# Kernel tuning notes

Hardware: AMD Instinct MI355X
Metric: run time of the kernel (lower is better)

Reference implementation:

```python
import jax, jax.numpy as jnp
import numpy as np

B, D, K = 32768, 512, 5
SIM_THRESH = 0.7
GATE_TEMP = 1.0
LN_EPS = 1e-5


def setup_inputs() -> dict:
    key = jax.random.key(0)
    ks = jax.random.split(key, 12)
    s = 1.0 / np.sqrt(D)
    query = jax.random.normal(ks[0], (B, D), dtype=jnp.float32)
    retrieved_memories = jax.random.normal(ks[1], (B, K, D), dtype=jnp.float32)
    similarities = jax.random.uniform(ks[2], (B, K), dtype=jnp.float32)
    mask = jax.random.randint(ks[3], (B, K), 0, 2) > 0
    mask = mask.at[:, 0].set(True)  # at least one valid memory per row
    return {
        "query": query,
        "retrieved_memories": retrieved_memories,
        "similarities": similarities,
        "mask": mask,
        "Wq": jax.random.normal(ks[4], (D, D), dtype=jnp.float32) * s,
        "bq": jnp.zeros((D,), jnp.float32),
        "Wk": jax.random.normal(ks[5], (D, D), dtype=jnp.float32) * s,
        "bk": jnp.zeros((D,), jnp.float32),
        "Wv": jax.random.normal(ks[6], (D, D), dtype=jnp.float32) * s,
        "bv": jnp.zeros((D,), jnp.float32),
        "Wo": jax.random.normal(ks[7], (D, D), dtype=jnp.float32) * s,
        "bo": jnp.zeros((D,), jnp.float32),
        "Wg": jax.random.normal(ks[8], (2 * D, 1), dtype=jnp.float32) * s,
        "bg": jnp.zeros((1,), jnp.float32),
        "ln_g": jnp.ones((D,), jnp.float32),
        "ln_b": jnp.zeros((D,), jnp.float32),
    }


def reference(query, retrieved_memories, similarities, mask,
              Wq, bq, Wk, bk, Wv, bv, Wo, bo, Wg, bg, ln_g, ln_b):
    scale = D ** (-0.5)
    q = query @ Wq + bq                                          # (B, D)
    k = jnp.einsum('bkd,de->bke', retrieved_memories, Wk) + bk   # (B, K, D)
    v = jnp.einsum('bkd,de->bke', retrieved_memories, Wv) + bv   # (B, K, D)
    scores = jnp.einsum('bd,bkd->bk', q, k) * scale              # (B, K)
    scores = jnp.where(mask, scores, -jnp.inf)
    w = jax.nn.softmax(scores, axis=-1)
    w = jnp.where(mask, w, 0.0)
    mem = jnp.einsum('bk,bkd->bd', w, v)                         # (B, D)
    mem = mem @ Wo + bo
    # gated fusion
    max_sim = jnp.max(similarities, axis=-1, keepdims=True)      # (B, 1)
    gate = jax.nn.sigmoid(jnp.concatenate([query, mem], axis=-1) @ Wg + bg)
    conf = jax.nn.sigmoid(GATE_TEMP * (max_sim - SIM_THRESH))
    out = query + (gate * conf) * mem
    # layer norm
    mu = jnp.mean(out, axis=-1, keepdims=True)
    var = jnp.mean((out - mu) ** 2, axis=-1, keepdims=True)
    out = (out - mu) * jax.lax.rsqrt(var + LN_EPS) * ln_g + ln_b
    return out
```

## Files before the change

### kernel.cpp

```cpp
#include <hip/hip_runtime.h>

#define DD 512
#define KM 5
#define B_ROWS 32768

typedef __attribute__((ext_vector_type(8))) short short8;
typedef __attribute__((ext_vector_type(4))) short s16x4;
typedef __attribute__((ext_vector_type(4))) float f32x4;

static __device__ __forceinline__ short f2bf(float x) {
  unsigned u = __builtin_bit_cast(unsigned, x);
  u = (u + 0x7fffu + ((u >> 16) & 1u)) >> 16;
  return (short)u;
}
static __device__ __forceinline__ float bf2f(short s) {
  unsigned u = ((unsigned)(unsigned short)s) << 16;
  return __builtin_bit_cast(float, u);
}

#define SYNC0() do { asm volatile("s_waitcnt vmcnt(0) lgkmcnt(0)" ::: "memory"); __builtin_amdgcn_s_barrier(); } while (0)
#define SYNC2() do { asm volatile("s_waitcnt vmcnt(2) lgkmcnt(0)" ::: "memory"); __builtin_amdgcn_s_barrier(); } while (0)
#define BAR_LGKM() do { asm volatile("s_waitcnt lgkmcnt(0)" ::: "memory"); __builtin_amdgcn_s_barrier(); } while (0)

__global__ __launch_bounds__(512, 2)
void prepG(const float* __restrict__ Wq, const float* __restrict__ bq,
           const float* __restrict__ Wk, const float* __restrict__ Wv,
           const float* __restrict__ Wo, const float* __restrict__ bo,
           const float* __restrict__ bv,
           short* __restrict__ At, short* __restrict__ Ct,
           float* __restrict__ w0, float* __restrict__ d0) {
  __shared__ short sh[12288];
  const int tid = threadIdx.x;
  const int blk = blockIdx.x;
  if (blk < 64) {
    const bool isC = blk >= 32;
    const int b = blk & 31;
    const int j0 = (b >> 3) * 128;
    const int i0 = (b & 7) * 64;
    const int lane = tid & 63;
    const int w = tid >> 6;
    const int wm = w & 1, wn = w >> 1;
    const int kg = lane >> 4, lr = lane & 15;
    const float* Ysrc = isC ? Wv : Wq;
    f32x4 acc[4] = {};
    f32x4 ra0, ra1;
    f32x4 rbv;
    if (!isC) {
      const float* p = Wk + (size_t)(j0 + (tid >> 2)) * DD + (tid & 3) * 8;
      ra0 = *(const f32x4*)p; ra1 = *(const f32x4*)(p + 4);
    } else {
      const float* p = Wo + (size_t)(tid >> 4) * DD + j0 + (tid & 15) * 8;
      ra0 = *(const f32x4*)p; ra1 = *(const f32x4*)(p + 4);
    }
    rbv = *(const f32x4*)(Ysrc + (size_t)(i0 + (tid >> 3)) * DD + (tid & 7) * 4);
    for (int ki = 0; ki < 16; ++ki) {
      short* As = (ki & 1) ? (sh + 4096) : sh;
      short* Bs = (ki & 1) ? (sh + 10240) : (sh + 8192);
      if (!isC) {
        short8 sv;
        sv[0]=f2bf(ra0[0]); sv[1]=f2bf(ra0[1]); sv[2]=f2bf(ra0[2]); sv[3]=f2bf(ra0[3]);
        sv[4]=f2bf(ra1[0]); sv[5]=f2bf(ra1[1]); sv[6]=f2bf(ra1[2]); sv[7]=f2bf(ra1[3]);
        *(short8*)&As[(tid >> 2) * 32 + (((tid & 3) * 8) ^ (((tid >> 2) & 3) << 3))] = sv;
      } else {
        const int e = tid >> 4;
#pragma unroll
        for (int c = 0; c < 8; ++c) {
          const int j = (tid & 15) * 8 + c;
          const float v = (c < 4) ? ra0[c & 3] : ra1[c & 3];
          As[j * 32 + (e ^ ((j & 3) << 3))] = f2bf(v);
        }
      }
      {
        s16x4 sv;
        sv[0]=f2bf(rbv[0]); sv[1]=f2bf(rbv[1]); sv[2]=f2bf(rbv[2]); sv[3]=f2bf(rbv[3]);
        *(s16x4*)&Bs[(tid >> 3) * 32 + (((tid & 7) * 4) ^ (((tid >> 3) & 3) << 3))] = sv;
      }
      if (ki < 15) {
        const int kt = (ki + 1) * 32;
        if (!isC) {
          const float* p = Wk + (size_t)(j0 + (tid >> 2)) * DD + kt + (tid & 3) * 8;
          ra0 = *(const f32x4*)p; ra1 = *(const f32x4*)(p + 4);
        } else {
          const float* p = Wo + (size_t)(kt + (tid >> 4)) * DD + j0 + (tid & 15) * 8;
          ra0 = *(const f32x4*)p; ra1 = *(const f32x4*)(p + 4);
        }
        rbv = *(const f32x4*)(Ysrc + (size_t)(i0 + (tid >> 3)) * DD + kt + (tid & 7) * 4);
      }
      __syncthreads();
      short8 av[4], bvv;
#pragma unroll
      for (int mi = 0; mi < 4; ++mi) {
        const int ar = wm * 64 + mi * 16 + lr;
        av[mi] = *(const short8*)&As[ar * 32 + ((kg * 8) ^ ((lr & 3) << 3))];
      }
      {
        const int br = wn * 16 + lr;
        bvv = *(const short8*)&Bs[br * 32 + ((kg * 8) ^ ((lr & 3) << 3))];
      }
#pragma unroll
      for (int mi = 0; mi < 4; ++mi)
        acc[mi] = __builtin_amdgcn_mfma_f32_16x16x32_bf16(av[mi], bvv, acc[mi], 0, 0, 0);
      __syncthreads();
    }
    short* P = isC ? Ct : At;
    const int col = i0 + wn * 16 + lr;
#pragma unroll
    for (int mi = 0; mi < 4; ++mi)
#pragma unroll
      for (int r = 0; r < 4; ++r)
        P[(size_t)(j0 + wm * 64 + mi * 16 + kg * 4 + r) * DD + col] = f2bf(acc[mi][r]);
  } else if (blk < 128) {
    const int j = (blk - 64) * 8 + (tid >> 6);
    const int lane = tid & 63;
    const float* r = Wk + (size_t)j * DD + lane * 8;
    f32x4 a = *(const f32x4*)r;
    f32x4 c = *(const f32x4*)(r + 4);
    const float* bp = bq + lane * 8;
    f32x4 ba = *(const f32x4*)bp;
    f32x4 bc = *(const f32x4*)(bp + 4);
    float s = a[0]*ba[0] + a[1]*ba[1] + a[2]*ba[2] + a[3]*ba[3]
            + c[0]*bc[0] + c[1]*bc[1] + c[2]*bc[2] + c[3]*bc[3];
#pragma unroll
    for (int off = 32; off > 0; off >>= 1) s += __shfl_xor(s, off);
    if (lane == 0) w0[j] = s;
  } else {
    float* red = (float*)sh;
    const int j = (blk - 128) * 256 + (tid & 255);
    const int half = tid >> 8;
    float s = 0.f;
    for (int e = half * 256; e < half * 256 + 256; ++e)
      s += bv[e] * Wo[(size_t)e * DD + j];
    red[half * 256 + (tid & 255)] = s;
    __syncthreads();
    if (half == 0) d0[j] = red[tid] + red[256 + tid] + bo[j];
  }
}

#define STAGE_W(MAT, TI, DST) do {                                                 \
  _Pragma("unroll") for (int c = 0; c < 4; ++c) {                                  \
    const short* _src = (MAT) + (size_t)(c * 128 + (tid >> 2)) * DD + (TI) * 32    \
                        + (((tid & 3) * 8) ^ (((tid >> 2) & 3) << 3));             \
    __builtin_amdgcn_global_load_lds(                                              \
        (const __attribute__((address_space(1))) void*)_src,                       \
        (__attribute__((address_space(3))) void*)(&(DST)[c * 4096 + w * 512]),     \
        16, 0, 0);                                                                 \
  } } while (0)

#define WRITE_A(DST, QLO, QHI) do {                                                \
  short8 _sv;                                                                      \
  _sv[0]=f2bf((QLO)[0]); _sv[1]=f2bf((QLO)[1]); _sv[2]=f2bf((QLO)[2]); _sv[3]=f2bf((QLO)[3]); \
  _sv[4]=f2bf((QHI)[0]); _sv[5]=f2bf((QHI)[1]); _sv[6]=f2bf((QHI)[2]); _sv[7]=f2bf((QHI)[3]); \
  *(short8*)&(DST)[arow * 32 + (acol ^ ((arow & 3) << 3))] = _sv; } while (0)

#define ROW_FINISH(SV, MA, MC, VM, ROW)                                     \
    {                                                                       \
      float mx = -1e30f;                                                    \
      _Pragma("unroll") for (int k = 0; k < KM; ++k)                        \
        if ((VM) & (1 << k)) mx = fmaxf(mx, SV[k]);                         \
      float wk[KM]; float sum = 0.f;                                        \
      _Pragma("unroll") for (int k = 0; k < KM; ++k) {                      \
        wk[k] = ((VM) & (1 << k)) ? __expf(SV[k] - mx) : 0.f;               \
        sum += wk[k];                                                       \
      }                                                                     \
      const float inv = 1.f / sum;                                          \
      float o[8] = {0.f,0.f,0.f,0.f,0.f,0.f,0.f,0.f};                       \
      _Pragma("unroll") for (int k = 0; k < KM; ++k)                        \
        if ((VM) & (1 << k)) {                                              \
          const float g = wk[k] * inv;                                      \
          _Pragma("unroll") for (int i = 0; i < 4; ++i) {                   \
            o[i] += g * MA[k][i]; o[4 + i] += g * MC[k][i];                 \
          }                                                                 \
        }                                                                   \
      short8 ov;                                                            \
      _Pragma("unroll") for (int i = 0; i < 8; ++i) ov[i] = f2bf(o[i]);     \
      *(short8*)&R1[((ROW) * DD + lane * 8) ^ (((ROW) & 7) << 3)] = ov;     \
    }

__global__ __launch_bounds__(512, 2)
void mk(const float* __restrict__ q, const short* __restrict__ Atw,
        const float* __restrict__ w0, const float* __restrict__ mem,
        const int* __restrict__ mask, const short* __restrict__ Ctw,
        const float* __restrict__ d0, const float* __restrict__ sims,
        const float* __restrict__ Wg, const float* __restrict__ bgp,
        const float* __restrict__ lng, const float* __restrict__ lnb,
        float* __restrict__ outp) {
  __shared__ short R1[128 * DD];
  __shared__ short RS[DD * 32];
  const int tid = threadIdx.x;
  const int lane = tid & 63;
  const int w = tid >> 6;
  const int kg = lane >> 4, lr = lane & 15;
  const int bm = blockIdx.x;

  short* As0 = R1;
  short* As1 = R1 + 4096;
  short* RS1 = R1 + 8192;

  f32x4 acc[8][4] = {};
  const int arow = tid >> 2, acol = (tid & 3) * 8;
  const float* qbase = q + (size_t)(bm * 128 + arow) * DD + acol;
  {
    STAGE_W(Atw, 0, RS);
    __builtin_amdgcn_sched_barrier(0);
    f32x4 q0a = *(const f32x4*)qbase;
    f32x4 q0b = *(const f32x4*)(qbase + 4);
    WRITE_A(As0, q0a, q0b);
    f32x4 qA = *(const f32x4*)(qbase + 32);
    f32x4 qB = *(const f32x4*)(qbase + 36);
    SYNC2();
    for (int ki = 0; ki < 16; ++ki) {
      const short* Asc = (ki & 1) ? As1 : As0;
      short* Asn = (ki & 1) ? As0 : As1;
      const short* RSc = (ki & 1) ? RS1 : RS;
      short* RSn = (ki & 1) ? RS : RS1;
      short8 av[8], bvv[4];
#pragma unroll
      for (int mi = 0; mi < 8; ++mi) {
        const int ar = mi * 16 + lr;
        av[mi] = *(const short8*)&Asc[ar * 32 + ((kg * 8) ^ ((lr & 3) << 3))];
      }
#pragma unroll
      for (int ni = 0; ni < 4; ++ni) {
        const int row = w * 64 + ni * 16 + lr;
        bvv[ni] = *(const short8*)&RSc[row * 32 + ((kg * 8) ^ ((lr & 3) << 3))];
      }
      if (ki < 15) {
        WRITE_A(Asn, qA, qB);
        STAGE_W(Atw, ki + 1, RSn);
        __builtin_amdgcn_sched_barrier(0);
        if (ki < 14) {
          qA = *(const f32x4*)(qbase + (ki + 2) * 32);
          qB = *(const f32x4*)(qbase + (ki + 2) * 32 + 4);
        }
      }
#pragma unroll
      for (int mi = 0; mi < 8; ++mi)
#pragma unroll
        for (int ni = 0; ni < 4; ++ni)
          acc[mi][ni] = __builtin_amdgcn_mfma_f32_16x16x32_bf16(av[mi], bvv[ni], acc[mi][ni], 0, 0, 0);
      if (ki < 14) { SYNC2(); } else { SYNC0(); }
    }
  }
#pragma unroll
  for (int ni = 0; ni < 4; ++ni) {
    const int col = w * 64 + ni * 16 + lr;
    const float b0 = w0[col];
#pragma unroll
    for (int mi = 0; mi < 8; ++mi)
#pragma unroll
      for (int r = 0; r < 4; ++r)
        R1[(mi * 16 + kg * 4 + r) * DD + col] = f2bf(acc[mi][ni][r] + b0);
  }
  BAR_LGKM();
  STAGE_W(Ctw, 0, RS);
  const float scale = 0.044194173824159216f;
  for (int rr = 0; rr < 16; rr += 2) {
    const int row0 = w * 16 + rr;
    const size_t b0 = (size_t)bm * 128 + row0;
    const short8 tv0 = *(const short8*)&R1[row0 * DD + lane * 8];
    const short8 tv1 = *(const short8*)&R1[(row0 + 1) * DD + lane * 8];
    float tf0[8], tf1[8];
#pragma unroll
    for (int i = 0; i < 8; ++i) { tf0[i] = bf2f(tv0[i]); tf1[i] = bf2f(tv1[i]); }
    int vm0 = 0, vm1 = 0;
#pragma unroll
    for (int k = 0; k < KM; ++k) {
      vm0 |= (__builtin_amdgcn_readfirstlane(mask[b0 * KM + k]) ? 1 : 0) << k;
      vm1 |= (__builtin_amdgcn_readfirstlane(mask[(b0 + 1) * KM + k]) ? 1 : 0) << k;
    }
    f32x4 ma0[KM], mc0[KM], ma1[KM], mc1[KM];
#pragma unroll
    for (int k = 0; k < KM; ++k) {
      if (vm0 & (1 << k)) {
        const f32x4* mp = (const f32x4*)(mem + (b0 * KM + k) * DD + lane * 8);
        ma0[k] = __builtin_nontemporal_load(mp);
        mc0[k] = __builtin_nontemporal_load(mp + 1);
      }
      if (vm1 & (1 << k)) {
        const f32x4* mp = (const f32x4*)(mem + ((b0 + 1) * KM + k) * DD + lane * 8);
        ma1[k] = __builtin_nontemporal_load(mp);
        mc1[k] = __builtin_nontemporal_load(mp + 1);
      }
    }
    float s0[KM], s1[KM];
#pragma unroll
    for (int k = 0; k < KM; ++k) {
      if (vm0 & (1 << k)) {
        float p = 0.f;
#pragma unroll
        for (int i = 0; i < 4; ++i) { p += tf0[i] * ma0[k][i]; p += tf0[4 + i] * mc0[k][i]; }
#pragma unroll
        for (int off = 32; off > 0; off >>= 1) p += __shfl_xor(p, off);
        s0[k] = p * scale;
      }
      if (vm1 & (1 << k)) {
        float p = 0.f;
#pragma unroll
        for (int i = 0; i < 4; ++i) { p += tf1[i] * ma1[k][i]; p += tf1[4 + i] * mc1[k][i]; }
#pragma unroll
        for (int off = 32; off > 0; off >>= 1) p += __shfl_xor(p, off);
        s1[k] = p * scale;
      }
    }
    ROW_FINISH(s0, ma0, mc0, vm0, row0)
    ROW_FINISH(s1, ma1, mc1, vm1, (row0 + 1))
  }
  SYNC0();
  f32x4 acc2[8][4] = {};
  for (int ki = 0; ki < 16; ++ki) {
    short8 av[8], bvv[4];
#pragma unroll
    for (int mi = 0; mi < 8; ++mi) {
      const int ar = mi * 16 + lr;
      av[mi] = *(const short8*)&R1[(ar * DD + ki * 32 + kg * 8) ^ ((ar & 7) << 3)];
    }
#pragma unroll
    for (int ni = 0; ni < 4; ++ni) {
      const int row = w * 64 + ni * 16 + lr;
      bvv[ni] = *(const short8*)&RS[row * 32 + ((kg * 8) ^ ((lr & 3) << 3))];
    }
    BAR_LGKM();
    if (ki < 15) STAGE_W(Ctw, ki + 1, RS);
#pragma unroll
    for (int mi = 0; mi < 8; ++mi)
#pragma unroll
      for (int ni = 0; ni < 4; ++ni)
        acc2[mi][ni] = __builtin_amdgcn_mfma_f32_16x16x32_bf16(av[mi], bvv[ni], acc2[mi][ni], 0, 0, 0);
    SYNC0();
  }
#pragma unroll
  for (int ni = 0; ni < 4; ++ni) {
    const int col = w * 64 + ni * 16 + lr;
    const float b0 = d0[col];
#pragma unroll
    for (int mi = 0; mi < 8; ++mi)
#pragma unroll
      for (int r = 0; r < 4; ++r)
        R1[(mi * 16 + kg * 4 + r) * DD + col] = f2bf(acc2[mi][ni][r] + b0);
  }
  BAR_LGKM();
  {
    const float* wg1 = Wg + lane * 8;
    const float* wg2 = Wg + DD + lane * 8;
    f32x4 g1a = *(const f32x4*)wg1, g1b = *(const f32x4*)(wg1 + 4);
    f32x4 g2a = *(const f32x4*)wg2, g2b = *(const f32x4*)(wg2 + 4);
    f32x4 la = *(const f32x4*)(lng + lane * 8), lb4 = *(const f32x4*)(lng + lane * 8 + 4);
    f32x4 ba = *(const f32x4*)(lnb + lane * 8), bb4 = *(const f32x4*)(lnb + lane * 8 + 4);
    const float bgs = bgp[0];
    for (int rr = 0; rr < 16; ++rr) {
      const int row = w * 16 + rr;
      const size_t b = (size_t)bm * 128 + row;
      const float* qp = q + b * DD + lane * 8;
      f32x4 q0 = *(const f32x4*)qp;
      f32x4 q1 = *(const f32x4*)(qp + 4);
      float qf[8] = {q0[0],q0[1],q0[2],q0[3],q1[0],q1[1],q1[2],q1[3]};
      const short8 mv = *(const short8*)&R1[row * DD + lane * 8];
      float mf[8];
#pragma unroll
      for (int i = 0; i < 8; ++i) mf[i] = bf2f(mv[i]);
      float gp = qf[0]*g1a[0]+qf[1]*g1a[1]+qf[2]*g1a[2]+qf[3]*g1a[3]
               + qf[4]*g1b[0]+qf[5]*g1b[1]+qf[6]*g1b[2]+qf[7]*g1b[3]
               + mf[0]*g2a[0]+mf[1]*g2a[1]+mf[2]*g2a[2]+mf[3]*g2a[3]
               + mf[4]*g2b[0]+mf[5]*g2b[1]+mf[6]*g2b[2]+mf[7]*g2b[3];
#pragma unroll
      for (int off = 32; off > 0; off >>= 1) gp += __shfl_xor(gp, off);
      const float gate = 1.f / (1.f + __expf(-(gp + bgs)));
      float ms = sims[b * KM];
#pragma unroll
      for (int k = 1; k < KM; ++k) ms = fmaxf(ms, sims[b * KM + k]);
      const float conf = 1.f / (1.f + __expf(-(ms - 0.7f)));
      const float gc = gate * conf;
      float o[8];
      float s1 = 0.f, s2 = 0.f;
#pragma unroll
      for (int i = 0; i < 8; ++i) {
        o[i] = qf[i] + gc * mf[i];
        s1 += o[i];
        s2 += o[i] * o[i];
      }
#pragma unroll
      for (int off = 32; off > 0; off >>= 1) { s1 += __shfl_xor(s1, off); s2 += __shfl_xor(s2, off); }
      const float mu = s1 * (1.f / 512.f);
      const float var = s2 * (1.f / 512.f) - mu * mu;
      const float rs = rsqrtf(var + 1e-5f);
      f32x4 r0, r1;
#pragma unroll
      for (int i = 0; i < 4; ++i) r0[i] = (o[i] - mu) * rs * la[i] + ba[i];
#pragma unroll
      for (int i = 0; i < 4; ++i) r1[i] = (o[4 + i] - mu) * rs * lb4[i] + bb4[i];
      float* op = outp + b * DD + lane * 8;
      __builtin_nontemporal_store(r0, (f32x4*)op);
      __builtin_nontemporal_store(r1, (f32x4*)(op + 4));
    }
  }
}

extern "C" void kernel_launch(void* const* d_in, const int* in_sizes, int n_in,
                              void* d_out, int out_size, void* d_ws, size_t ws_size,
                              hipStream_t stream) {
  const float* query = (const float*)d_in[0];
  const float* mem   = (const float*)d_in[1];
  const float* sims  = (const float*)d_in[2];
  const int*   mask  = (const int*)d_in[3];
  const float* Wq = (const float*)d_in[4];
  const float* bq = (const float*)d_in[5];
  const float* Wk = (const float*)d_in[6];
  const float* Wv = (const float*)d_in[8];
  const float* bv = (const float*)d_in[9];
  const float* Wo = (const float*)d_in[10];
  const float* bo = (const float*)d_in[11];
  const float* Wg = (const float*)d_in[12];
  const float* bg = (const float*)d_in[13];
  const float* ln_g = (const float*)d_in[14];
  const float* ln_b = (const float*)d_in[15];
  float* out = (float*)d_out;

  char* ws = (char*)d_ws;
  short* At = (short*)ws;
  short* Ct = At + (size_t)DD * DD;
  float* w0 = (float*)(Ct + (size_t)DD * DD);
  float* d0 = w0 + DD;

  prepG<<<dim3(130), dim3(512), 0, stream>>>(Wq, bq, Wk, Wv, Wo, bo, bv, At, Ct, w0, d0);
  mk<<<dim3(B_ROWS / 128), dim3(512), 0, stream>>>(query, At, w0, mem, mask,
                                                   Ct, d0, sims, Wg, bg, ln_g, ln_b, out);
}
```

Measured before the change: 147.6 us.

## Load B weight fragments directly from global into registers, drop LDS staging

The prep kernel now writes the precomputed At/Ct weight products in a K-tiled packed layout, so each lane's MFMA B fragment is one contiguous 16-byte global load. The main kernel drops the RS LDS buffer and the global_load_lds staging. Instead it double-buffers B fragments in registers, with loops unrolled in pairs, and uses lighter LDS-only barriers. This removes LDS traffic and vmcnt waits for the weights, but relies on L2/L1 hits for the repeated weight reads across blocks and raises register pressure.

```diff
diff --git a/kernel.cpp b/kernel.cpp
--- a/kernel.cpp
+++ b/kernel.cpp
@@ -18,8 +18,6 @@
   return __builtin_bit_cast(float, u);
 }
 
-#define SYNC0() do { asm volatile("s_waitcnt vmcnt(0) lgkmcnt(0)" ::: "memory"); __builtin_amdgcn_s_barrier(); } while (0)
-#define SYNC2() do { asm volatile("s_waitcnt vmcnt(2) lgkmcnt(0)" ::: "memory"); __builtin_amdgcn_s_barrier(); } while (0)
 #define BAR_LGKM() do { asm volatile("s_waitcnt lgkmcnt(0)" ::: "memory"); __builtin_amdgcn_s_barrier(); } while (0)
 
 __global__ __launch_bounds__(512, 2)
@@ -103,12 +101,16 @@
       __syncthreads();
     }
     short* P = isC ? Ct : At;
-    const int col = i0 + wn * 16 + lr;
+    const int cwl = wn * 16 + lr;
+    const int kiv = (b & 7) * 2 + (cwl >> 5);
+    const int kkv = cwl & 31;
 #pragma unroll
     for (int mi = 0; mi < 4; ++mi)
 #pragma unroll
-      for (int r = 0; r < 4; ++r)
-        P[(size_t)(j0 + wm * 64 + mi * 16 + kg * 4 + r) * DD + col] = f2bf(acc[mi][r]);
+      for (int r = 0; r < 4; ++r) {
+        const int j = j0 + wm * 64 + mi * 16 + kg * 4 + r;
+        P[(size_t)kiv * 16384 + j * 32 + kkv] = f2bf(acc[mi][r]);
+      }
   } else if (blk < 128) {
     const int j = (blk - 64) * 8 + (tid >> 6);
     const int lane = tid & 63;
@@ -136,21 +138,47 @@
   }
 }
 
-#define STAGE_W(MAT, TI, DST) do {                                                 \
-  _Pragma("unroll") for (int c = 0; c < 4; ++c) {                                  \
-    const short* _src = (MAT) + (size_t)(c * 128 + (tid >> 2)) * DD + (TI) * 32    \
-                        + (((tid & 3) * 8) ^ (((tid >> 2) & 3) << 3));             \
-    __builtin_amdgcn_global_load_lds(                                              \
-        (const __attribute__((address_space(1))) void*)_src,                       \
-        (__attribute__((address_space(3))) void*)(&(DST)[c * 4096 + w * 512]),     \
-        16, 0, 0);                                                                 \
-  } } while (0)
-
 #define WRITE_A(DST, QLO, QHI) do {                                                \
   short8 _sv;                                                                      \
   _sv[0]=f2bf((QLO)[0]); _sv[1]=f2bf((QLO)[1]); _sv[2]=f2bf((QLO)[2]); _sv[3]=f2bf((QLO)[3]); \
   _sv[4]=f2bf((QHI)[0]); _sv[5]=f2bf((QHI)[1]); _sv[6]=f2bf((QHI)[2]); _sv[7]=f2bf((QHI)[3]); \
   *(short8*)&(DST)[arow * 32 + (acol ^ ((arow & 3) << 3))] = _sv; } while (0)
+
+#define G1ITER(KI, ASC, ASN, BC, BN) do {                                   \
+    short8 av[8];                                                           \
+    _Pragma("unroll") for (int mi = 0; mi < 8; ++mi) {                      \
+      const int ar = mi * 16 + lr;                                          \
+      av[mi] = *(const short8*)&(ASC)[ar * 32 + ((kg * 8) ^ ((lr & 3) << 3))]; \
+    }                                                                       \
+    if ((KI) < 15) { WRITE_A(ASN, qA, qB); }                                \
+    if ((KI) < 15) {                                                        \
+      _Pragma("unroll") for (int ni = 0; ni < 4; ++ni)                      \
+        (BN)[ni] = *(const short8*)(atb + ((KI) + 1) * 16384 + ni * 512);   \
+    }                                                                       \
+    if ((KI) < 14) {                                                        \
+      qA = *(const f32x4*)(qbase + ((KI) + 2) * 32);                        \
+      qB = *(const f32x4*)(qbase + ((KI) + 2) * 32 + 4);                    \
+    }                                                                       \
+    _Pragma("unroll") for (int mi = 0; mi < 8; ++mi)                        \
+      _Pragma("unroll") for (int ni = 0; ni < 4; ++ni)                      \
+        acc[mi][ni] = __builtin_amdgcn_mfma_f32_16x16x32_bf16(av[mi], (BC)[ni], acc[mi][ni], 0, 0, 0); \
+    BAR_LGKM();                                                             \
+  } while (0)
+
+#define G2ITER(KI, BC, BN) do {                                             \
+    short8 av[8];                                                           \
+    _Pragma("unroll") for (int mi = 0; mi < 8; ++mi) {                      \
+      const int ar = mi * 16 + lr;                                          \
+      av[mi] = *(const short8*)&R1[(ar * DD + (KI) * 32 + kg * 8) ^ ((ar & 7) << 3)]; \
+    }                                                                       \
+    if ((KI) < 15) {                                                        \
+      _Pragma("unroll") for (int ni = 0; ni < 4; ++ni)                      \
+        (BN)[ni] = *(const short8*)(ctb + ((KI) + 1) * 16384 + ni * 512);   \
+    }                                                                       \
+    _Pragma("unroll") for (int mi = 0; mi < 8; ++mi)                        \
+      _Pragma("unroll") for (int ni = 0; ni < 4; ++ni)                      \
+        acc2[mi][ni] = __builtin_amdgcn_mfma_f32_16x16x32_bf16(av[mi], (BC)[ni], acc2[mi][ni], 0, 0, 0); \
+  } while (0)
 
 #define ROW_FINISH(SV, MA, MC, VM, ROW)                                     \
     {                                                                       \
@@ -177,15 +205,14 @@
     }
 
 __global__ __launch_bounds__(512, 2)
-void mk(const float* __restrict__ q, const short* __restrict__ Atw,
+void mk(const float* __restrict__ q, const short* __restrict__ AtP,
         const float* __restrict__ w0, const float* __restrict__ mem,
-        const int* __restrict__ mask, const short* __restrict__ Ctw,
+        const int* __restrict__ mask, const short* __restrict__ CtP,
         const float* __restrict__ d0, const float* __restrict__ sims,
         const float* __restrict__ Wg, const float* __restrict__ bgp,
         const float* __restrict__ lng, const float* __restrict__ lnb,
         float* __restrict__ outp) {
   __shared__ short R1[128 * DD];
-  __shared__ short RS[DD * 32];
   const int tid = threadIdx.x;
   const int lane = tid & 63;
   const int w = tid >> 6;
@@ -194,51 +221,26 @@
 
   short* As0 = R1;
   short* As1 = R1 + 4096;
-  short* RS1 = R1 + 8192;
+
+  const short* atb = AtP + (size_t)(w * 64 + lr) * 32 + kg * 8;
+  const short* ctb = CtP + (size_t)(w * 64 + lr) * 32 + kg * 8;
 
   f32x4 acc[8][4] = {};
   const int arow = tid >> 2, acol = (tid & 3) * 8;
   const float* qbase = q + (size_t)(bm * 128 + arow) * DD + acol;
   {
-    STAGE_W(Atw, 0, RS);
-    __builtin_amdgcn_sched_barrier(0);
-    f32x4 q0a = *(const f32x4*)qbase;
-    f32x4 q0b = *(const f32x4*)(qbase + 4);
-    WRITE_A(As0, q0a, q0b);
-    f32x4 qA = *(const f32x4*)(qbase + 32);
-    f32x4 qB = *(const f32x4*)(qbase + 36);
-    SYNC2();
-    for (int ki = 0; ki < 16; ++ki) {
-      const short* Asc = (ki & 1) ? As1 : As0;
-      short* Asn = (ki & 1) ? As0 : As1;
-      const short* RSc = (ki & 1) ? RS1 : RS;
-      short* RSn = (ki & 1) ? RS : RS1;
-      short8 av[8], bvv[4];
-#pragma unroll
-      for (int mi = 0; mi < 8; ++mi) {
-        const int ar = mi * 16 + lr;
-        av[mi] = *(const short8*)&Asc[ar * 32 + ((kg * 8) ^ ((lr & 3) << 3))];
-      }
-#pragma unroll
-      for (int ni = 0; ni < 4; ++ni) {
-        const int row = w * 64 + ni * 16 + lr;
-        bvv[ni] = *(const short8*)&RSc[row * 32 + ((kg * 8) ^ ((lr & 3) << 3))];
-      }
-      if (ki < 15) {
-        WRITE_A(Asn, qA, qB);
-        STAGE_W(Atw, ki + 1, RSn);
-        __builtin_amdgcn_sched_barrier(0);
-        if (ki < 14) {
-          qA = *(const f32x4*)(qbase + (ki + 2) * 32);
-          qB = *(const f32x4*)(qbase + (ki + 2) * 32 + 4);
-        }
-      }
-#pragma unroll
-      for (int mi = 0; mi < 8; ++mi)
-#pragma unroll
-        for (int ni = 0; ni < 4; ++ni)
-          acc[mi][ni] = __builtin_amdgcn_mfma_f32_16x16x32_bf16(av[mi], bvv[ni], acc[mi][ni], 0, 0, 0);
-      if (ki < 14) { SYNC2(); } else { SYNC0(); }
+    f32x4 qA = *(const f32x4*)qbase;
+    f32x4 qB = *(const f32x4*)(qbase + 4);
+    WRITE_A(As0, qA, qB);
+    qA = *(const f32x4*)(qbase + 32);
+    qB = *(const f32x4*)(qbase + 36);
+    short8 bA[4], bB[4];
+#pragma unroll
+    for (int ni = 0; ni < 4; ++ni) bA[ni] = *(const short8*)(atb + ni * 512);
+    BAR_LGKM();
+    for (int kp = 0; kp < 8; ++kp) {
+      G1ITER(2 * kp,     As0, As1, bA, bB);
+      G1ITER(2 * kp + 1, As1, As0, bB, bA);
     }
   }
 #pragma unroll
@@ -252,7 +254,6 @@
         R1[(mi * 16 + kg * 4 + r) * DD + col] = f2bf(acc[mi][ni][r] + b0);
   }
   BAR_LGKM();
-  STAGE_W(Ctw, 0, RS);
   const float scale = 0.044194173824159216f;
   for (int rr = 0; rr < 16; rr += 2) {
     const int row0 = w * 16 + rr;
@@ -305,29 +306,18 @@
     ROW_FINISH(s0, ma0, mc0, vm0, row0)
     ROW_FINISH(s1, ma1, mc1, vm1, (row0 + 1))
   }
-  SYNC0();
+  BAR_LGKM();
   f32x4 acc2[8][4] = {};
-  for (int ki = 0; ki < 16; ++ki) {
-    short8 av[8], bvv[4];
-#pragma unroll
-    for (int mi = 0; mi < 8; ++mi) {
-      const int ar = mi * 16 + lr;
-      av[mi] = *(const short8*)&R1[(ar * DD + ki * 32 + kg * 8) ^ ((ar & 7) << 3)];
-    }
-#pragma unroll
-    for (int ni = 0; ni < 4; ++ni) {
-      const int row = w * 64 + ni * 16 + lr;
-      bvv[ni] = *(const short8*)&RS[row * 32 + ((kg * 8) ^ ((lr & 3) << 3))];
-    }
-    BAR_LGKM();
-    if (ki < 15) STAGE_W(Ctw, ki + 1, RS);
-#pragma unroll
-    for (int mi = 0; mi < 8; ++mi)
-#pragma unroll
-      for (int ni = 0; ni < 4; ++ni)
-        acc2[mi][ni] = __builtin_amdgcn_mfma_f32_16x16x32_bf16(av[mi], bvv[ni], acc2[mi][ni], 0, 0, 0);
-    SYNC0();
-  }
+  {
+    short8 cA[4], cB[4];
+#pragma unroll
+    for (int ni = 0; ni < 4; ++ni) cA[ni] = *(const short8*)(ctb + ni * 512);
+    for (int kp = 0; kp < 8; ++kp) {
+      G2ITER(2 * kp,     cA, cB);
+      G2ITER(2 * kp + 1, cB, cA);
+    }
+  }
+  BAR_LGKM();
 #pragma unroll
   for (int ni = 0; ni < 4; ++ni) {
     const int col = w * 64 + ni * 16 + lr;
@@ -416,12 +406,12 @@
   float* out = (float*)d_out;
 
   char* ws = (char*)d_ws;
-  short* At = (short*)ws;
-  short* Ct = At + (size_t)DD * DD;
-  float* w0 = (float*)(Ct + (size_t)DD * DD);
+  short* AtP = (short*)ws;
+  short* CtP = AtP + (size_t)DD * DD;
+  float* w0 = (float*)(CtP + (size_t)DD * DD);
   float* d0 = w0 + DD;
 
-  prepG<<<dim3(130), dim3(512), 0, stream>>>(Wq, bq, Wk, Wv, Wo, bo, bv, At, Ct, w0, d0);
-  mk<<<dim3(B_ROWS / 128), dim3(512), 0, stream>>>(query, At, w0, mem, mask,
-                                                   Ct, d0, sims, Wg, bg, ln_g, ln_b, out);
+  prepG<<<dim3(130), dim3(512), 0, stream>>>(Wq, bq, Wk, Wv, Wo, bo, bv, AtP, CtP, w0, d0);
+  mk<<<dim3(B_ROWS / 128), dim3(512), 0, stream>>>(query, AtP, w0, mem, mask,
+                                                   CtP, d0, sims, Wg, bg, ln_g, ln_b, out);
 }
```

Result: faster. 130.5 us, median of 2 (-11.5%).
